# Optimization experiments

Measured on AMD Instinct MI355X. Metric: run time of the kernel, lower is better.

## Reference

```python
import jax, jax.numpy as jnp
import numpy as np

B, T, I, H = 64, 2048, 512, 512


def setup_inputs() -> dict:
    key = jax.random.key(0)
    k0, k1, k2, k3, k4 = jax.random.split(key, 5)
    s = H ** -0.5
    return {
        "inputs": jax.random.normal(k0, (B, T, I), dtype=jnp.float32),
        "weights_i": jax.random.uniform(k1, (I, 4 * H), minval=-s, maxval=s, dtype=jnp.float32),
        "bias_i": jax.random.uniform(k2, (4 * H,), minval=-s, maxval=s, dtype=jnp.float32),
        "weights_h": jax.random.uniform(k3, (H, 4 * H), minval=-s, maxval=s, dtype=jnp.float32),
        "bias_h": jax.random.uniform(k4, (4 * H,), minval=-s, maxval=s, dtype=jnp.float32),
    }


def _lstm(inputs, weights_i, bias_i, weights_h, bias_h):
    hsz = weights_h.shape[0]
    b = inputs.shape[0]
    # Precompute input contribution for all timesteps: (B,T,4H)
    x_gates = jnp.einsum("bti,ig->btg", inputs, weights_i) + bias_i + bias_h
    x_gates = jnp.transpose(x_gates, (1, 0, 2))  # (T,B,4H)

    h0 = jnp.zeros((b, hsz), dtype=inputs.dtype)
    c0 = jnp.zeros((b, hsz), dtype=inputs.dtype)

    def step(carry, xg):
        h, c = carry
        g = xg + h @ weights_h  # (B,4H)
        i_t = jax.nn.sigmoid(g[:, 0 * hsz:1 * hsz])
        f_t = jax.nn.sigmoid(g[:, 1 * hsz:2 * hsz])
        g_t = jnp.tanh(g[:, 2 * hsz:3 * hsz])
        o_t = jax.nn.sigmoid(g[:, 3 * hsz:4 * hsz])
        c_new = f_t * c + i_t * g_t
        h_new = o_t * jnp.tanh(c_new)
        return (h_new, c_new), o_t  # original appends o_t as the per-step output

    (h_T, _), outs = jax.lax.scan(step, (h0, c0), x_gates)
    output = jnp.transpose(outs, (1, 0, 2))  # (B,T,H)
    return output, h_T


def reference(inputs, weights_i, bias_i, weights_h, bias_h):
    return _lstm(inputs, weights_i, bias_i, weights_h, bias_h)
```

## Files before the change

kernel.cpp:

```cpp
#include <hip/hip_runtime.h>
#include <stdint.h>

#define B_ 64
#define T_ 2048
#define I_ 512
#define H_ 512

typedef short bf16x8 __attribute__((ext_vector_type(8)));
typedef float f32x4 __attribute__((ext_vector_type(4)));

__device__ __forceinline__ unsigned short f2bf(float f) {
  union { float f; unsigned u; } x; x.f = f;
  unsigned r = x.u + 0x7fffu + ((x.u >> 16) & 1u);
  return (unsigned short)(r >> 16);
}
__device__ __forceinline__ float sigm(float x) { return 1.0f / (1.0f + __expf(-x)); }
__device__ __forceinline__ float tanhfast(float x) { return 1.0f - 2.0f / (__expf(2.0f * x) + 1.0f); }

__global__ void prep_kernel(const float* __restrict__ in, unsigned short* __restrict__ xbf,
                            unsigned int* __restrict__ flags) {
  int t = blockIdx.x;
  int tid = threadIdx.x;
  if (t == 0) {
    for (int i = tid; i < 1024; i += 256) flags[i] = 0u;
  }
  const int slab = B_ * I_;
  for (int idx = tid * 4; idx < slab; idx += 256 * 4) {
    int b = idx >> 9;
    int i = idx & 511;
    const float4 v = *reinterpret_cast<const float4*>(in + ((size_t)b * T_ + t) * I_ + i);
    ushort4 o;
    o.x = f2bf(v.x); o.y = f2bf(v.y); o.z = f2bf(v.z); o.w = f2bf(v.w);
    *reinterpret_cast<ushort4*>(xbf + (size_t)t * slab + idx) = o;
  }
}

#define APPLY16(M) M(0,"0") M(1,"64") M(2,"128") M(3,"192") M(4,"256") M(5,"320") \
  M(6,"384") M(7,"448") M(8,"512") M(9,"576") M(10,"640") M(11,"704") \
  M(12,"768") M(13,"832") M(14,"896") M(15,"960")

__global__ __launch_bounds__(64, 1) void lstm_kernel(
    const float* __restrict__ Wi, const float* __restrict__ bi,
    const float* __restrict__ Wh, const float* __restrict__ bh,
    const unsigned short* __restrict__ xbf,
    unsigned short* __restrict__ hbuf,
    unsigned int* flags,
    float* __restrict__ out, float* __restrict__ hT)
{
  const int wg = blockIdx.x;
  const int bg = wg >> 6;
  const int gc = wg & 63;
  const int lane = threadIdx.x;

  extern __shared__ char lds[];
  short* Wp = (short*)lds;
  float* gates = (float*)(lds + 65536);

  {
    const int n = lane & 31;
    const int col = ((n >> 3) << 9) + (gc << 3) + (n & 7);
    for (int kf = (lane >> 5); kf < 1024; kf += 2) {
      float v = (kf < 512) ? Wi[(size_t)kf * 2048 + col]
                           : Wh[(size_t)(kf - 512) * 2048 + col];
      int kk = kf >> 5;
      int lp = (((kf & 31) >> 3) << 4) + (n & 15);
      int tl = n >> 4;
      Wp[((((kk << 1) + tl) << 6) + lp) * 8 + (kf & 7)] = (short)f2bf(v);
    }
  }
  const int n0 = lane & 15;
  const int col0 = ((n0 >> 3) << 9) + (gc << 3) + (n0 & 7);
  const int n1 = n0 + 16;
  const int col1 = ((n1 >> 3) << 9) + (gc << 3) + (n1 & 7);
  const float rb0 = bi[col0] + bh[col0];
  const float rb1 = bi[col1] + bh[col1];
  __syncthreads();

  const int bbase = bg << 4;
  const size_t arow = ((size_t)(bbase + (lane & 15))) * 512 + ((lane >> 4) << 3);
  const short* wl = Wp + (lane << 3);
  const int jc = gc << 3;
  const int b_l = lane >> 2;
  const int j0 = (lane & 3) << 1;
  const int brow = bbase + b_l;

  float c0 = 0.f, c1 = 0.f;
  unsigned int* myflag = flags + wg;
  unsigned int* pollflag = flags + (bg << 6) + lane;

  bf16x8 xa[16];
  bf16x8 ha[16];

#define LDX(i, OFF) asm volatile("global_load_dwordx4 %0, %1, off offset:" OFF \
    : "=v"(xa[i]) : "v"(xsrc) : "memory");
#define LDH(i, OFF) asm volatile("global_load_dwordx4 %0, %1, off offset:" OFF " sc0 sc1" \
    : "=v"(ha[i]) : "v"(hsrc) : "memory");

  {
    const unsigned short* xsrc = xbf + arow;
    APPLY16(LDX)
  }
  asm volatile("s_waitcnt vmcnt(0)" ::: "memory");
  __builtin_amdgcn_sched_barrier(0);

  for (int t = 0; t < T_; ++t) {
    f32x4 acc0 = {rb0, rb0, rb0, rb0};
    f32x4 acc1 = {rb1, rb1, rb1, rb1};

#pragma unroll
    for (int kk = 0; kk < 16; ++kk) {
      bf16x8 w0 = *reinterpret_cast<const bf16x8*>(wl + (kk << 10));
      bf16x8 w1 = *reinterpret_cast<const bf16x8*>(wl + (kk << 10) + 512);
      acc0 = __builtin_amdgcn_mfma_f32_16x16x32_bf16(xa[kk], w0, acc0, 0, 0, 0);
      acc1 = __builtin_amdgcn_mfma_f32_16x16x32_bf16(xa[kk], w1, acc1, 0, 0, 0);
    }
    __builtin_amdgcn_sched_barrier(0);

    {
      const int tn = (t + 1 < T_) ? t + 1 : t;
      const unsigned short* xsrc = xbf + (size_t)tn * (B_ * I_) + arow;
      APPLY16(LDX)
    }

    if (t > 0) {
      const unsigned int want = (unsigned int)t;
      while (__hip_atomic_load(pollflag, __ATOMIC_RELAXED, __HIP_MEMORY_SCOPE_AGENT) < want) {}
      asm volatile("" ::: "memory");

      {
        const unsigned short* hsrc = hbuf + (size_t)(t & 1) * (B_ * H_) + arow;
        APPLY16(LDH)
      }
      asm volatile("s_waitcnt vmcnt(0)" ::: "memory");
      __builtin_amdgcn_sched_barrier(0);
#pragma unroll
      for (int kk = 0; kk < 16; ++kk) {
        bf16x8 w0 = *reinterpret_cast<const bf16x8*>(wl + ((kk + 16) << 10));
        bf16x8 w1 = *reinterpret_cast<const bf16x8*>(wl + ((kk + 16) << 10) + 512);
        acc0 = __builtin_amdgcn_mfma_f32_16x16x32_bf16(ha[kk], w0, acc0, 0, 0, 0);
        acc1 = __builtin_amdgcn_mfma_f32_16x16x32_bf16(ha[kk], w1, acc1, 0, 0, 0);
      }
    }

    {
      const int cc = lane & 15;
      const int rb = (lane >> 4) << 2;
#pragma unroll
      for (int r = 0; r < 4; ++r) {
        gates[(rb + r) * 32 + cc] = acc0[r];
        gates[(rb + r) * 32 + 16 + cc] = acc1[r];
      }
    }
    __syncthreads();
    const float* grow = gates + b_l * 32;
    float gi0 = grow[j0],      gi1 = grow[j0 + 1];
    float gf0 = grow[8 + j0],  gf1 = grow[9 + j0];
    float gg0 = grow[16 + j0], gg1 = grow[17 + j0];
    float go0 = grow[24 + j0], go1 = grow[25 + j0];
    __syncthreads();
    float o0 = sigm(go0), o1 = sigm(go1);
    c0 = sigm(gf0) * c0 + sigm(gi0) * tanhfast(gg0);
    c1 = sigm(gf1) * c1 + sigm(gi1) * tanhfast(gg1);
    float h0 = o0 * tanhfast(c0);
    float h1 = o1 * tanhfast(c1);

    unsigned int hpack = (unsigned int)f2bf(h0) | ((unsigned int)f2bf(h1) << 16);
    unsigned int* hw = (unsigned int*)(hbuf + (size_t)((t + 1) & 1) * (B_ * H_) + (size_t)brow * H_ + jc + j0);
    __hip_atomic_store(hw, hpack, __ATOMIC_RELAXED, __HIP_MEMORY_SCOPE_AGENT);
    asm volatile("s_waitcnt vmcnt(0)" ::: "memory");
    if (lane == 0 && t < T_ - 1)
      __hip_atomic_store(myflag, (unsigned int)(t + 1), __ATOMIC_RELAXED, __HIP_MEMORY_SCOPE_AGENT);

    float* orow = out + ((size_t)brow * T_ + t) * H_ + jc + j0;
    orow[0] = o0; orow[1] = o1;
    if (t == T_ - 1) {
      float* hTo = hT + (size_t)brow * H_ + jc + j0;
      hTo[0] = h0; hTo[1] = h1;
    }
  }
#undef LDX
#undef LDH
}

extern "C" void kernel_launch(void* const* d_in, const int* in_sizes, int n_in,
                              void* d_out, int out_size, void* d_ws, size_t ws_size,
                              hipStream_t stream) {
  const float* inputs = (const float*)d_in[0];
  const float* Wi = (const float*)d_in[1];
  const float* bi = (const float*)d_in[2];
  const float* Wh = (const float*)d_in[3];
  const float* bh = (const float*)d_in[4];
  float* out = (float*)d_out;
  float* hT = out + (size_t)B_ * T_ * H_;

  unsigned int* flags = (unsigned int*)d_ws;
  unsigned short* hbuf = (unsigned short*)((char*)d_ws + 16384);
  unsigned short* xbf = (unsigned short*)((char*)d_ws + 16384 + 2 * B_ * H_ * 2);

  (void)hipFuncSetAttribute((const void*)lstm_kernel,
                            hipFuncAttributeMaxDynamicSharedMemorySize, 67584);

  prep_kernel<<<dim3(T_), dim3(256), 0, stream>>>(inputs, xbf, flags);
  lstm_kernel<<<dim3(256), dim3(64), 67584, stream>>>(Wi, bi, Wh, bh, xbf, hbuf, flags, out, hT);
}
```

Measured before the change: 7.506 ms.

## Use per-step atomic counters and wider per-workgroup tiles for the recurrent LSTM

Cuts the workgroup count from 256 to 128, and each workgroup now computes all four gates for 16 hidden columns. The LSTM cell update therefore runs in registers, with no LDS gate exchange and no __syncthreads. The per-workgroup flag polling, in which each lane reads a different flag, is replaced by a single per-timestep, per-batch-group atomic counter that all 32 producers increment. The h loads are issued before the x-part MFMAs so that their latency overlaps that compute. The cost is twice the LDS weight footprint per workgroup (128KB), a larger counter array, and contention on a shared atomic.

```diff
diff --git a/kernel.cpp b/kernel.cpp
--- a/kernel.cpp
+++ b/kernel.cpp
@@ -5,6 +5,8 @@
 #define T_ 2048
 #define I_ 512
 #define H_ 512
+#define NG 4
+#define WPG 32
 
 typedef short bf16x8 __attribute__((ext_vector_type(8)));
 typedef float f32x4 __attribute__((ext_vector_type(4)));
@@ -18,12 +20,11 @@
 __device__ __forceinline__ float tanhfast(float x) { return 1.0f - 2.0f / (__expf(2.0f * x) + 1.0f); }
 
 __global__ void prep_kernel(const float* __restrict__ in, unsigned short* __restrict__ xbf,
-                            unsigned int* __restrict__ flags) {
+                            unsigned int* __restrict__ ctr) {
   int t = blockIdx.x;
   int tid = threadIdx.x;
-  if (t == 0) {
-    for (int i = tid; i < 1024; i += 256) flags[i] = 0u;
-  }
+  for (int i = tid; i < 64; i += 256) ctr[t * 64 + i] = 0u;
+  if (t == 0) for (int i = tid; i < 64; i += 256) ctr[2048 * 64 + i] = 0u;
   const int slab = B_ * I_;
   for (int idx = tid * 4; idx < slab; idx += 256 * 4) {
     int b = idx >> 9;
@@ -44,49 +45,48 @@
     const float* __restrict__ Wh, const float* __restrict__ bh,
     const unsigned short* __restrict__ xbf,
     unsigned short* __restrict__ hbuf,
-    unsigned int* flags,
+    unsigned int* ctr,
     float* __restrict__ out, float* __restrict__ hT)
 {
   const int wg = blockIdx.x;
-  const int bg = wg >> 6;
-  const int gc = wg & 63;
+  const int bg = wg >> 5;
+  const int gc = wg & 31;
   const int lane = threadIdx.x;
 
   extern __shared__ char lds[];
   short* Wp = (short*)lds;
-  float* gates = (float*)(lds + 65536);
 
   {
-    const int n = lane & 31;
-    const int col = ((n >> 3) << 9) + (gc << 3) + (n & 7);
-    for (int kf = (lane >> 5); kf < 1024; kf += 2) {
-      float v = (kf < 512) ? Wi[(size_t)kf * 2048 + col]
-                           : Wh[(size_t)(kf - 512) * 2048 + col];
-      int kk = kf >> 5;
-      int lp = (((kf & 31) >> 3) << 4) + (n & 15);
-      int tl = n >> 4;
-      Wp[((((kk << 1) + tl) << 6) + lp) * 8 + (kf & 7)] = (short)f2bf(v);
-    }
-  }
-  const int n0 = lane & 15;
-  const int col0 = ((n0 >> 3) << 9) + (gc << 3) + (n0 & 7);
-  const int n1 = n0 + 16;
-  const int col1 = ((n1 >> 3) << 9) + (gc << 3) + (n1 & 7);
-  const float rb0 = bi[col0] + bh[col0];
-  const float rb1 = bi[col1] + bh[col1];
-  __syncthreads();
+    const int q = lane >> 4, j = lane & 15;
+    const int col = (q << 9) + (gc << 4) + j;
+    for (int kf = 0; kf < 512; ++kf) {
+      float v = Wi[(size_t)kf * 2048 + col];
+      const int kk = kf >> 5;
+      const int lp = (((kf & 31) >> 3) << 4) + j;
+      Wp[((((kk << 2) + q) << 6) + lp) * 8 + (kf & 7)] = (short)f2bf(v);
+    }
+    for (int kf = 512; kf < 1024; ++kf) {
+      float v = Wh[(size_t)(kf - 512) * 2048 + col];
+      const int kk = kf >> 5;
+      const int lp = (((kf & 31) >> 3) << 4) + j;
+      Wp[((((kk << 2) + q) << 6) + lp) * 8 + (kf & 7)] = (short)f2bf(v);
+    }
+  }
+  const int jj = lane & 15;
+  float rb[4];
+#pragma unroll
+  for (int q = 0; q < 4; ++q) {
+    const int col = (q << 9) + (gc << 4) + jj;
+    rb[q] = bi[col] + bh[col];
+  }
 
   const int bbase = bg << 4;
-  const size_t arow = ((size_t)(bbase + (lane & 15))) * 512 + ((lane >> 4) << 3);
+  const size_t arow = ((size_t)(bbase + jj)) * 512 + ((lane >> 4) << 3);
   const short* wl = Wp + (lane << 3);
-  const int jc = gc << 3;
-  const int b_l = lane >> 2;
-  const int j0 = (lane & 3) << 1;
-  const int brow = bbase + b_l;
-
-  float c0 = 0.f, c1 = 0.f;
-  unsigned int* myflag = flags + wg;
-  unsigned int* pollflag = flags + (bg << 6) + lane;
+  const int hcol = (gc << 4) + jj;
+  const int rowb = bbase + ((lane >> 4) << 2);
+
+  float c[4] = {0.f, 0.f, 0.f, 0.f};
 
   bf16x8 xa[16];
   bf16x8 ha[16];
@@ -104,15 +104,27 @@
   __builtin_amdgcn_sched_barrier(0);
 
   for (int t = 0; t < T_; ++t) {
-    f32x4 acc0 = {rb0, rb0, rb0, rb0};
-    f32x4 acc1 = {rb1, rb1, rb1, rb1};
+    f32x4 acc[4];
+#pragma unroll
+    for (int q = 0; q < 4; ++q) acc[q] = (f32x4){rb[q], rb[q], rb[q], rb[q]};
+
+    if (t > 0) {
+      while (__hip_atomic_load(ctr + ((size_t)t * NG + bg) * 16,
+                               __ATOMIC_RELAXED, __HIP_MEMORY_SCOPE_AGENT) < WPG) {}
+      asm volatile("" ::: "memory");
+      const unsigned short* hsrc = hbuf + (size_t)(t & 1) * (B_ * H_) + arow;
+      APPLY16(LDH)
+      __builtin_amdgcn_sched_barrier(0);
+    }
 
 #pragma unroll
     for (int kk = 0; kk < 16; ++kk) {
-      bf16x8 w0 = *reinterpret_cast<const bf16x8*>(wl + (kk << 10));
-      bf16x8 w1 = *reinterpret_cast<const bf16x8*>(wl + (kk << 10) + 512);
-      acc0 = __builtin_amdgcn_mfma_f32_16x16x32_bf16(xa[kk], w0, acc0, 0, 0, 0);
-      acc1 = __builtin_amdgcn_mfma_f32_16x16x32_bf16(xa[kk], w1, acc1, 0, 0, 0);
+      const short* wk = wl + (kk << 11);
+#pragma unroll
+      for (int q = 0; q < 4; ++q) {
+        bf16x8 w = *reinterpret_cast<const bf16x8*>(wk + (q << 9));
+        acc[q] = __builtin_amdgcn_mfma_f32_16x16x32_bf16(xa[kk], w, acc[q], 0, 0, 0);
+      }
     }
     __builtin_amdgcn_sched_barrier(0);
 
@@ -123,60 +135,50 @@
     }
 
     if (t > 0) {
-      const unsigned int want = (unsigned int)t;
-      while (__hip_atomic_load(pollflag, __ATOMIC_RELAXED, __HIP_MEMORY_SCOPE_AGENT) < want) {}
-      asm volatile("" ::: "memory");
-
-      {
-        const unsigned short* hsrc = hbuf + (size_t)(t & 1) * (B_ * H_) + arow;
-        APPLY16(LDH)
+      asm volatile("s_waitcnt vmcnt(16)" ::: "memory");
+      __builtin_amdgcn_sched_barrier(0);
+#pragma unroll
+      for (int kk = 0; kk < 16; ++kk) {
+        const short* wk = wl + ((kk + 16) << 11);
+#pragma unroll
+        for (int q = 0; q < 4; ++q) {
+          bf16x8 w = *reinterpret_cast<const bf16x8*>(wk + (q << 9));
+          acc[q] = __builtin_amdgcn_mfma_f32_16x16x32_bf16(ha[kk], w, acc[q], 0, 0, 0);
+        }
       }
-      asm volatile("s_waitcnt vmcnt(0)" ::: "memory");
-      __builtin_amdgcn_sched_barrier(0);
-#pragma unroll
-      for (int kk = 0; kk < 16; ++kk) {
-        bf16x8 w0 = *reinterpret_cast<const bf16x8*>(wl + ((kk + 16) << 10));
-        bf16x8 w1 = *reinterpret_cast<const bf16x8*>(wl + ((kk + 16) << 10) + 512);
-        acc0 = __builtin_amdgcn_mfma_f32_16x16x32_bf16(ha[kk], w0, acc0, 0, 0, 0);
-        acc1 = __builtin_amdgcn_mfma_f32_16x16x32_bf16(ha[kk], w1, acc1, 0, 0, 0);
+    }
+
+    unsigned short* hwb = hbuf + (size_t)((t + 1) & 1) * (B_ * H_);
+    float osave[4];
+#pragma unroll
+    for (int r = 0; r < 4; ++r) {
+      float gi = acc[0][r], gf = acc[1][r], gg = acc[2][r], go = acc[3][r];
+      float ot = sigm(go);
+      c[r] = sigm(gf) * c[r] + sigm(gi) * tanhfast(gg);
+      float h = ot * tanhfast(c[r]);
+      osave[r] = ot;
+      unsigned int hd = (unsigned int)f2bf(h);
+      const unsigned short* hp = hwb + (size_t)(rowb + r) * H_ + hcol;
+      asm volatile("global_store_short %0, %1, off sc0 sc1" :: "v"(hp), "v"(hd) : "memory");
+    }
+    if (t == T_ - 1) {
+#pragma unroll
+      for (int r = 0; r < 4; ++r) {
+        float ot = osave[r];
+        float h = ot * tanhfast(c[r]);
+        hT[(size_t)(rowb + r) * H_ + hcol] = h;
       }
     }
 
-    {
-      const int cc = lane & 15;
-      const int rb = (lane >> 4) << 2;
-#pragma unroll
-      for (int r = 0; r < 4; ++r) {
-        gates[(rb + r) * 32 + cc] = acc0[r];
-        gates[(rb + r) * 32 + 16 + cc] = acc1[r];
-      }
-    }
-    __syncthreads();
-    const float* grow = gates + b_l * 32;
-    float gi0 = grow[j0],      gi1 = grow[j0 + 1];
-    float gf0 = grow[8 + j0],  gf1 = grow[9 + j0];
-    float gg0 = grow[16 + j0], gg1 = grow[17 + j0];
-    float go0 = grow[24 + j0], go1 = grow[25 + j0];
-    __syncthreads();
-    float o0 = sigm(go0), o1 = sigm(go1);
-    c0 = sigm(gf0) * c0 + sigm(gi0) * tanhfast(gg0);
-    c1 = sigm(gf1) * c1 + sigm(gi1) * tanhfast(gg1);
-    float h0 = o0 * tanhfast(c0);
-    float h1 = o1 * tanhfast(c1);
-
-    unsigned int hpack = (unsigned int)f2bf(h0) | ((unsigned int)f2bf(h1) << 16);
-    unsigned int* hw = (unsigned int*)(hbuf + (size_t)((t + 1) & 1) * (B_ * H_) + (size_t)brow * H_ + jc + j0);
-    __hip_atomic_store(hw, hpack, __ATOMIC_RELAXED, __HIP_MEMORY_SCOPE_AGENT);
     asm volatile("s_waitcnt vmcnt(0)" ::: "memory");
-    if (lane == 0 && t < T_ - 1)
-      __hip_atomic_store(myflag, (unsigned int)(t + 1), __ATOMIC_RELAXED, __HIP_MEMORY_SCOPE_AGENT);
-
-    float* orow = out + ((size_t)brow * T_ + t) * H_ + jc + j0;
-    orow[0] = o0; orow[1] = o1;
-    if (t == T_ - 1) {
-      float* hTo = hT + (size_t)brow * H_ + jc + j0;
-      hTo[0] = h0; hTo[1] = h1;
-    }
+    __builtin_amdgcn_sched_barrier(0);
+    if (lane == 0)
+      __hip_atomic_fetch_add(ctr + ((size_t)(t + 1) * NG + bg) * 16, 1u,
+                             __ATOMIC_RELAXED, __HIP_MEMORY_SCOPE_AGENT);
+
+#pragma unroll
+    for (int r = 0; r < 4; ++r)
+      out[((size_t)(rowb + r) * T_ + t) * H_ + hcol] = osave[r];
   }
 #undef LDX
 #undef LDH
@@ -193,13 +195,13 @@
   float* out = (float*)d_out;
   float* hT = out + (size_t)B_ * T_ * H_;
 
-  unsigned int* flags = (unsigned int*)d_ws;
-  unsigned short* hbuf = (unsigned short*)((char*)d_ws + 16384);
-  unsigned short* xbf = (unsigned short*)((char*)d_ws + 16384 + 2 * B_ * H_ * 2);
+  unsigned int* ctr = (unsigned int*)d_ws;
+  unsigned short* hbuf = (unsigned short*)((char*)d_ws + 524544);
+  unsigned short* xbf = (unsigned short*)((char*)d_ws + 524544 + 131072);
 
   (void)hipFuncSetAttribute((const void*)lstm_kernel,
-                            hipFuncAttributeMaxDynamicSharedMemorySize, 67584);
-
-  prep_kernel<<<dim3(T_), dim3(256), 0, stream>>>(inputs, xbf, flags);
-  lstm_kernel<<<dim3(256), dim3(64), 67584, stream>>>(Wi, bi, Wh, bh, xbf, hbuf, flags, out, hT);
-}
+                            hipFuncAttributeMaxDynamicSharedMemorySize, 131072);
+
+  prep_kernel<<<dim3(T_), dim3(256), 0, stream>>>(inputs, xbf, ctr);
+  lstm_kernel<<<dim3(128), dim3(64), 131072, stream>>>(Wi, bi, Wh, bh, xbf, hbuf, ctr, out, hT);
+}
```

New measurement: 9.431 ms. 1.26x slower.

## Use per-step atomic counters, register-resident weights, and early h prefetch

Applied to the files above, without the earlier changes.

Replaces the per-workgroup monotonic flags, where each lane polls one of 64 flags, with a single per-timestep, per-batch-group atomic counter that each workgroup increments. The wait for it and the h-state loads are moved ahead of the x-projection MFMAs so those loads overlap that compute. All 64 weight fragments are held in VGPRs instead of being reread from LDS each step, which uses a large share of the register file and risks spills. Output stores are vectorised to float2, and the workspace layout grows to hold the counter array.

```diff
diff --git a/kernel.cpp b/kernel.cpp
--- a/kernel.cpp
+++ b/kernel.cpp
@@ -5,6 +5,8 @@
 #define T_ 2048
 #define I_ 512
 #define H_ 512
+#define NG 4
+#define WPG 64
 
 typedef short bf16x8 __attribute__((ext_vector_type(8)));
 typedef float f32x4 __attribute__((ext_vector_type(4)));
@@ -18,12 +20,11 @@
 __device__ __forceinline__ float tanhfast(float x) { return 1.0f - 2.0f / (__expf(2.0f * x) + 1.0f); }
 
 __global__ void prep_kernel(const float* __restrict__ in, unsigned short* __restrict__ xbf,
-                            unsigned int* __restrict__ flags) {
+                            unsigned int* __restrict__ ctr) {
   int t = blockIdx.x;
   int tid = threadIdx.x;
-  if (t == 0) {
-    for (int i = tid; i < 1024; i += 256) flags[i] = 0u;
-  }
+  for (int i = tid; i < 64; i += 256) ctr[t * 64 + i] = 0u;
+  if (t == 0) for (int i = tid; i < 64; i += 256) ctr[2048 * 64 + i] = 0u;
   const int slab = B_ * I_;
   for (int idx = tid * 4; idx < slab; idx += 256 * 4) {
     int b = idx >> 9;
@@ -44,7 +45,7 @@
     const float* __restrict__ Wh, const float* __restrict__ bh,
     const unsigned short* __restrict__ xbf,
     unsigned short* __restrict__ hbuf,
-    unsigned int* flags,
+    unsigned int* ctr,
     float* __restrict__ out, float* __restrict__ hT)
 {
   const int wg = blockIdx.x;
@@ -76,17 +77,20 @@
   const float rb1 = bi[col1] + bh[col1];
   __syncthreads();
 
+  const short* wl = Wp + (lane << 3);
+  bf16x8 wreg[64];
+#pragma unroll
+  for (int f = 0; f < 64; ++f)
+    wreg[f] = *reinterpret_cast<const bf16x8*>(wl + (f << 9));
+
   const int bbase = bg << 4;
   const size_t arow = ((size_t)(bbase + (lane & 15))) * 512 + ((lane >> 4) << 3);
-  const short* wl = Wp + (lane << 3);
   const int jc = gc << 3;
   const int b_l = lane >> 2;
   const int j0 = (lane & 3) << 1;
   const int brow = bbase + b_l;
 
   float c0 = 0.f, c1 = 0.f;
-  unsigned int* myflag = flags + wg;
-  unsigned int* pollflag = flags + (bg << 6) + lane;
 
   bf16x8 xa[16];
   bf16x8 ha[16];
@@ -107,12 +111,19 @@
     f32x4 acc0 = {rb0, rb0, rb0, rb0};
     f32x4 acc1 = {rb1, rb1, rb1, rb1};
 
+    if (t > 0) {
+      while (__hip_atomic_load(ctr + ((size_t)t * NG + bg) * 16,
+                               __ATOMIC_RELAXED, __HIP_MEMORY_SCOPE_AGENT) < WPG) {}
+      asm volatile("" ::: "memory");
+      const unsigned short* hsrc = hbuf + (size_t)(t & 1) * (B_ * H_) + arow;
+      APPLY16(LDH)
+      __builtin_amdgcn_sched_barrier(0);
+    }
+
 #pragma unroll
     for (int kk = 0; kk < 16; ++kk) {
-      bf16x8 w0 = *reinterpret_cast<const bf16x8*>(wl + (kk << 10));
-      bf16x8 w1 = *reinterpret_cast<const bf16x8*>(wl + (kk << 10) + 512);
-      acc0 = __builtin_amdgcn_mfma_f32_16x16x32_bf16(xa[kk], w0, acc0, 0, 0, 0);
-      acc1 = __builtin_amdgcn_mfma_f32_16x16x32_bf16(xa[kk], w1, acc1, 0, 0, 0);
+      acc0 = __builtin_amdgcn_mfma_f32_16x16x32_bf16(xa[kk], wreg[2 * kk],     acc0, 0, 0, 0);
+      acc1 = __builtin_amdgcn_mfma_f32_16x16x32_bf16(xa[kk], wreg[2 * kk + 1], acc1, 0, 0, 0);
     }
     __builtin_amdgcn_sched_barrier(0);
 
@@ -123,22 +134,12 @@
     }
 
     if (t > 0) {
-      const unsigned int want = (unsigned int)t;
-      while (__hip_atomic_load(pollflag, __ATOMIC_RELAXED, __HIP_MEMORY_SCOPE_AGENT) < want) {}
-      asm volatile("" ::: "memory");
-
-      {
-        const unsigned short* hsrc = hbuf + (size_t)(t & 1) * (B_ * H_) + arow;
-        APPLY16(LDH)
-      }
-      asm volatile("s_waitcnt vmcnt(0)" ::: "memory");
+      asm volatile("s_waitcnt vmcnt(16)" ::: "memory");
       __builtin_amdgcn_sched_barrier(0);
 #pragma unroll
       for (int kk = 0; kk < 16; ++kk) {
-        bf16x8 w0 = *reinterpret_cast<const bf16x8*>(wl + ((kk + 16) << 10));
-        bf16x8 w1 = *reinterpret_cast<const bf16x8*>(wl + ((kk + 16) << 10) + 512);
-        acc0 = __builtin_amdgcn_mfma_f32_16x16x32_bf16(ha[kk], w0, acc0, 0, 0, 0);
-        acc1 = __builtin_amdgcn_mfma_f32_16x16x32_bf16(ha[kk], w1, acc1, 0, 0, 0);
+        acc0 = __builtin_amdgcn_mfma_f32_16x16x32_bf16(ha[kk], wreg[32 + 2 * kk],     acc0, 0, 0, 0);
+        acc1 = __builtin_amdgcn_mfma_f32_16x16x32_bf16(ha[kk], wreg[32 + 2 * kk + 1], acc1, 0, 0, 0);
       }
     }
 
@@ -168,14 +169,16 @@
     unsigned int* hw = (unsigned int*)(hbuf + (size_t)((t + 1) & 1) * (B_ * H_) + (size_t)brow * H_ + jc + j0);
     __hip_atomic_store(hw, hpack, __ATOMIC_RELAXED, __HIP_MEMORY_SCOPE_AGENT);
     asm volatile("s_waitcnt vmcnt(0)" ::: "memory");
-    if (lane == 0 && t < T_ - 1)
-      __hip_atomic_store(myflag, (unsigned int)(t + 1), __ATOMIC_RELAXED, __HIP_MEMORY_SCOPE_AGENT);
-
-    float* orow = out + ((size_t)brow * T_ + t) * H_ + jc + j0;
-    orow[0] = o0; orow[1] = o1;
+    __builtin_amdgcn_sched_barrier(0);
+    if (lane == 0)
+      __hip_atomic_fetch_add(ctr + ((size_t)(t + 1) * NG + bg) * 16, 1u,
+                             __ATOMIC_RELAXED, __HIP_MEMORY_SCOPE_AGENT);
+
+    float2 ov = {o0, o1};
+    *reinterpret_cast<float2*>(out + ((size_t)brow * T_ + t) * H_ + jc + j0) = ov;
     if (t == T_ - 1) {
-      float* hTo = hT + (size_t)brow * H_ + jc + j0;
-      hTo[0] = h0; hTo[1] = h1;
+      float2 hv = {h0, h1};
+      *reinterpret_cast<float2*>(hT + (size_t)brow * H_ + jc + j0) = hv;
     }
   }
 #undef LDX
@@ -193,13 +196,13 @@
   float* out = (float*)d_out;
   float* hT = out + (size_t)B_ * T_ * H_;
 
-  unsigned int* flags = (unsigned int*)d_ws;
-  unsigned short* hbuf = (unsigned short*)((char*)d_ws + 16384);
-  unsigned short* xbf = (unsigned short*)((char*)d_ws + 16384 + 2 * B_ * H_ * 2);
+  unsigned int* ctr = (unsigned int*)d_ws;
+  unsigned short* hbuf = (unsigned short*)((char*)d_ws + 524544);
+  unsigned short* xbf = (unsigned short*)((char*)d_ws + 524544 + 131072);
 
   (void)hipFuncSetAttribute((const void*)lstm_kernel,
                             hipFuncAttributeMaxDynamicSharedMemorySize, 67584);
 
-  prep_kernel<<<dim3(T_), dim3(256), 0, stream>>>(inputs, xbf, flags);
-  lstm_kernel<<<dim3(256), dim3(64), 67584, stream>>>(Wi, bi, Wh, bh, xbf, hbuf, flags, out, hT);
-}
+  prep_kernel<<<dim3(T_), dim3(256), 0, stream>>>(inputs, xbf, ctr);
+  lstm_kernel<<<dim3(256), dim3(64), 67584, stream>>>(Wi, bi, Wh, bh, xbf, hbuf, ctr, out, hT);
+}
```

After: 7.109 ms. 1.06x faster.
